# Optimization experiments

Measured on AMD Instinct MI355X. Metric: run time of the kernel, lower is better.

Reference implementation:

```python
import jax, jax.numpy as jnp
import numpy as np

NEG = -100000.0  # matches torch masked_fill constant

def setup_inputs() -> dict:
    key = jax.random.key(0)
    k1, k2, k3, k4 = jax.random.split(key, 4)
    B, T, D, H, S = 8, 2048, 1024, 8, 128
    features = jax.random.normal(k1, (B, T, D), dtype=jnp.float32)
    begins = jax.random.randint(k2, (B, S), 0, 2016, dtype=jnp.int64)
    widths = jax.random.randint(k3, (B, S), 1, 33, dtype=jnp.int64)
    ends = jnp.minimum(begins + widths, T)
    key_w = jax.random.normal(k4, (H, D), dtype=jnp.float32) / np.sqrt(D)
    key_b = jnp.zeros((H,), dtype=jnp.float32)
    return {"features": features, "begins": begins, "ends": ends,
            "key_w": key_w, "key_b": key_b}


def reference(features, begins, ends, key_w, key_b):
    # features: [B, T, D]; begins/ends: [B, S]
    B, T, D = features.shape
    H = key_w.shape[0]
    S = begins.shape[1]
    pos = jnp.arange(T)  # [T]
    # span mask [B, S, T]
    mask = (begins[..., None] <= pos) & (pos < ends[..., None])
    # key projection: [B, T, H]
    logits = jnp.einsum('btd,hd->bth', features, key_w) + key_b
    # masked softmax over T per (batch, span, head): [B, S, T, H]
    masked = jnp.where(mask[..., None], logits[:, None, :, :], NEG)
    weights = jax.nn.softmax(masked, axis=-2)
    # values = features reshaped to heads: [B, T, H, D//H]
    values = features.reshape(B, T, H, D // H)
    res = jnp.einsum('bthd,bsth->bshd', values, weights)  # [B, S, H, D//H]
    return res.reshape(B, S, D)
```

## Files before the change

kernel.cpp:

```cpp
#include <hip/hip_runtime.h>

#define B_  8
#define T_  2048
#define D_  1024
#define H_  8
#define S_  128

__global__ __launch_bounds__(256) void logits_kernel(
    const float* __restrict__ feat,
    const float* __restrict__ kw,
    const float* __restrict__ kb,
    float* __restrict__ logits)
{
    const int wave = threadIdx.x >> 6;
    const int lane = threadIdx.x & 63;
    const int row0 = (blockIdx.x * 4 + wave) * 8;

    float acc[64];
#pragma unroll
    for (int j = 0; j < 64; ++j) acc[j] = 0.f;

#pragma unroll
    for (int c = 0; c < 4; ++c) {
        float4 kf[H_];
#pragma unroll
        for (int h = 0; h < H_; ++h)
            kf[h] = *(const float4*)(kw + h * D_ + c * 256 + lane * 4);
#pragma unroll
        for (int r = 0; r < 8; ++r) {
            float4 fv = *(const float4*)(feat + (size_t)(row0 + r) * D_ + c * 256 + lane * 4);
#pragma unroll
            for (int h = 0; h < H_; ++h)
                acc[r * 8 + h] += fv.x * kf[h].x + fv.y * kf[h].y
                                + fv.z * kf[h].z + fv.w * kf[h].w;
        }
    }

#pragma unroll
    for (int s = 0; s < 6; ++s) {
        const int m = 1 << s;
        const bool hi = (lane >> s) & 1;
#pragma unroll
        for (int j = 0; j < (32 >> s); ++j) {
            float mine  = hi ? acc[2 * j + 1] : acc[2 * j];
            float other = hi ? acc[2 * j]     : acc[2 * j + 1];
            acc[j] = mine + __shfl_xor(other, m, 64);
        }
    }

    logits[(size_t)row0 * H_ + lane] = acc[0] + kb[lane & 7];
}

__global__ __launch_bounds__(256) void pool_kernel(
    const float* __restrict__ feat,
    const int* __restrict__ begins,
    const int* __restrict__ ends,
    const float* __restrict__ logits,
    float* __restrict__ out)
{
    const int bs   = blockIdx.x;
    const int wv   = threadIdx.x >> 6;
    const int lane = threadIdx.x & 63;
    const int b    = bs >> 7;

    const int begin = begins[bs];
    const int width = ends[bs] - begin;
    const size_t row0 = (size_t)b * T_ + begin;

    float4 lv = *(const float4*)(logits + row0 * H_ + lane * 4);
    const int w8 = width * H_;
    float v0 = (4 * lane + 0 < w8) ? lv.x : -1e30f;
    float v1 = (4 * lane + 1 < w8) ? lv.y : -1e30f;
    float v2 = (4 * lane + 2 < w8) ? lv.z : -1e30f;
    float v3 = (4 * lane + 3 < w8) ? lv.w : -1e30f;

    float m0 = v0, m1 = v1, m2 = v2, m3 = v3;
#pragma unroll
    for (int off = 2; off <= 32; off <<= 1) {
        m0 = fmaxf(m0, __shfl_xor(m0, off, 64));
        m1 = fmaxf(m1, __shfl_xor(m1, off, 64));
        m2 = fmaxf(m2, __shfl_xor(m2, off, 64));
        m3 = fmaxf(m3, __shfl_xor(m3, off, 64));
    }

    float e0 = __expf(v0 - m0);
    float e1 = __expf(v1 - m1);
    float e2 = __expf(v2 - m2);
    float e3 = __expf(v3 - m3);
    float s0 = e0, s1 = e1, s2 = e2, s3 = e3;
#pragma unroll
    for (int off = 2; off <= 32; off <<= 1) {
        s0 += __shfl_xor(s0, off, 64);
        s1 += __shfl_xor(s1, off, 64);
        s2 += __shfl_xor(s2, off, 64);
        s3 += __shfl_xor(s3, off, 64);
    }
    const float w0 = e0 / s0, w1 = e1 / s1, w2 = e2 / s2, w3 = e3 / s3;

    const int p = wv >> 1;
    const float wlo = (wv & 1) ? w2 : w0;
    const float whi = (wv & 1) ? w3 : w1;
    const bool hiHalf = (lane >= 32);

    const int colbase = wv * 256 + lane * 4;
    const float* fbase = feat + row0 * D_ + colbase;

    float4 acc = make_float4(0.f, 0.f, 0.f, 0.f);
    const int nch = (width + 7) >> 3;
    for (int ch = 0; ch < nch; ++ch) {
#pragma unroll
        for (int k = 0; k < 8; ++k) {
            const int i = ch * 8 + k;
            const float t0 = __shfl(wlo, 2 * i + p, 64);
            const float t1 = __shfl(whi, 2 * i + p, 64);
            const float wt = hiHalf ? t1 : t0;
            const float4 fv = *(const float4*)(fbase + (size_t)i * D_);
            acc.x += wt * fv.x;
            acc.y += wt * fv.y;
            acc.z += wt * fv.z;
            acc.w += wt * fv.w;
        }
    }

    *(float4*)(out + (size_t)bs * D_ + colbase) = acc;
}

extern "C" void kernel_launch(void* const* d_in, const int* in_sizes, int n_in,
                              void* d_out, int out_size, void* d_ws, size_t ws_size,
                              hipStream_t stream) {
    const float* feat   = (const float*)d_in[0];
    const int*   begins = (const int*)d_in[1];
    const int*   ends   = (const int*)d_in[2];
    const float* kw     = (const float*)d_in[3];
    const float* kb     = (const float*)d_in[4];
    float*       out    = (float*)d_out;
    float* logits = (float*)d_ws;

    logits_kernel<<<(B_ * T_) / 32, 256, 0, stream>>>(feat, kw, kb, logits);
    pool_kernel<<<B_ * S_, 256, 0, stream>>>(feat, begins, ends, logits, out);
}
```

Before: 115.5 us.

## Fuse span logits computation into pooling kernel, computing logits only for span rows

```diff
diff --git a/kernel.cpp b/kernel.cpp
--- a/kernel.cpp
+++ b/kernel.cpp
@@ -6,20 +6,30 @@
 #define H_  8
 #define S_  128
 
-__global__ __launch_bounds__(256) void logits_kernel(
+__global__ __launch_bounds__(256) void pooler_fused(
     const float* __restrict__ feat,
+    const int* __restrict__ begins,
+    const int* __restrict__ ends,
     const float* __restrict__ kw,
     const float* __restrict__ kb,
-    float* __restrict__ logits)
+    float* __restrict__ out)
 {
-    const int wave = threadIdx.x >> 6;
+    const int bs   = blockIdx.x;
+    const int wv   = threadIdx.x >> 6;
     const int lane = threadIdx.x & 63;
-    const int row0 = (blockIdx.x * 4 + wave) * 8;
+    const int b    = bs >> 7;
+
+    const int begin = begins[bs];
+    const int width = ends[bs] - begin;
+    const size_t row0 = (size_t)b * T_ + begin;
+
+    __shared__ __align__(16) float lg[32 * H_];
 
     float acc[64];
 #pragma unroll
     for (int j = 0; j < 64; ++j) acc[j] = 0.f;
 
+    const int r0 = wv * 8;
 #pragma unroll
     for (int c = 0; c < 4; ++c) {
         float4 kf[H_];
@@ -28,7 +38,7 @@
             kf[h] = *(const float4*)(kw + h * D_ + c * 256 + lane * 4);
 #pragma unroll
         for (int r = 0; r < 8; ++r) {
-            float4 fv = *(const float4*)(feat + (size_t)(row0 + r) * D_ + c * 256 + lane * 4);
+            float4 fv = *(const float4*)(feat + (row0 + r0 + r) * D_ + c * 256 + lane * 4);
 #pragma unroll
             for (int h = 0; h < H_; ++h)
                 acc[r * 8 + h] += fv.x * kf[h].x + fv.y * kf[h].y
@@ -48,26 +58,10 @@
         }
     }
 
-    logits[(size_t)row0 * H_ + lane] = acc[0] + kb[lane & 7];
-}
+    lg[wv * 64 + lane] = acc[0] + kb[lane & 7];
+    __syncthreads();
 
-__global__ __launch_bounds__(256) void pool_kernel(
-    const float* __restrict__ feat,
-    const int* __restrict__ begins,
-    const int* __restrict__ ends,
-    const float* __restrict__ logits,
-    float* __restrict__ out)
-{
-    const int bs   = blockIdx.x;
-    const int wv   = threadIdx.x >> 6;
-    const int lane = threadIdx.x & 63;
-    const int b    = bs >> 7;
-
-    const int begin = begins[bs];
-    const int width = ends[bs] - begin;
-    const size_t row0 = (size_t)b * T_ + begin;
-
-    float4 lv = *(const float4*)(logits + row0 * H_ + lane * 4);
+    float4 lv = *(const float4*)&lg[lane * 4];
     const int w8 = width * H_;
     float v0 = (4 * lane + 0 < w8) ? lv.x : -1e30f;
     float v1 = (4 * lane + 1 < w8) ? lv.y : -1e30f;
@@ -105,7 +99,7 @@
     const int colbase = wv * 256 + lane * 4;
     const float* fbase = feat + row0 * D_ + colbase;
 
-    float4 acc = make_float4(0.f, 0.f, 0.f, 0.f);
+    float4 oacc = make_float4(0.f, 0.f, 0.f, 0.f);
     const int nch = (width + 7) >> 3;
     for (int ch = 0; ch < nch; ++ch) {
 #pragma unroll
@@ -115,14 +109,14 @@
             const float t1 = __shfl(whi, 2 * i + p, 64);
             const float wt = hiHalf ? t1 : t0;
             const float4 fv = *(const float4*)(fbase + (size_t)i * D_);
-            acc.x += wt * fv.x;
-            acc.y += wt * fv.y;
-            acc.z += wt * fv.z;
-            acc.w += wt * fv.w;
+            oacc.x += wt * fv.x;
+            oacc.y += wt * fv.y;
+            oacc.z += wt * fv.z;
+            oacc.w += wt * fv.w;
         }
     }
 
-    *(float4*)(out + (size_t)bs * D_ + colbase) = acc;
+    *(float4*)(out + (size_t)bs * D_ + colbase) = oacc;
 }
 
 extern "C" void kernel_launch(void* const* d_in, const int* in_sizes, int n_in,
@@ -134,8 +128,7 @@
     const float* kw     = (const float*)d_in[3];
     const float* kb     = (const float*)d_in[4];
     float*       out    = (float*)d_out;
-    float* logits = (float*)d_ws;
+    (void)d_ws; (void)ws_size;
 
-    logits_kernel<<<(B_ * T_) / 32, 256, 0, stream>>>(feat, kw, kb, logits);
-    pool_kernel<<<B_ * S_, 256, 0, stream>>>(feat, begins, ends, logits, out);
+    pooler_fused<<<B_ * S_, 256, 0, stream>>>(feat, begins, ends, kw, kb, out);
 }
```

Result: no change. 116.4 us (+0.8%).

## Stage key weights in LDS and assign one row per wave in logits kernel

Applied to the files above, without the earlier changes.

```diff
diff --git a/kernel.cpp b/kernel.cpp
--- a/kernel.cpp
+++ b/kernel.cpp
@@ -6,49 +6,64 @@
 #define H_  8
 #define S_  128
 
-__global__ __launch_bounds__(256) void logits_kernel(
+__global__ __launch_bounds__(1024) void logits_kernel(
     const float* __restrict__ feat,
     const float* __restrict__ kw,
     const float* __restrict__ kb,
     float* __restrict__ logits)
 {
-    const int wave = threadIdx.x >> 6;
+    const int wv   = threadIdx.x >> 6;
     const int lane = threadIdx.x & 63;
-    const int row0 = (blockIdx.x * 4 + wave) * 8;
+    const int row  = blockIdx.x * 16 + wv;
 
-    float acc[64];
+    __shared__ __align__(16) float kwl[H_ * D_];
+
+    {
+        const float4* src = (const float4*)kw;
+        float4*       dst = (float4*)kwl;
+        dst[threadIdx.x]        = src[threadIdx.x];
+        dst[threadIdx.x + 1024] = src[threadIdx.x + 1024];
+    }
+
+    const float* fr = feat + (size_t)row * D_;
+    float4 fv0 = *(const float4*)(fr +   0 + lane * 4);
+    float4 fv1 = *(const float4*)(fr + 256 + lane * 4);
+    float4 fv2 = *(const float4*)(fr + 512 + lane * 4);
+    float4 fv3 = *(const float4*)(fr + 768 + lane * 4);
+
+    __syncthreads();
+
+    float acc[H_];
 #pragma unroll
-    for (int j = 0; j < 64; ++j) acc[j] = 0.f;
-
-#pragma unroll
-    for (int c = 0; c < 4; ++c) {
-        float4 kf[H_];
-#pragma unroll
-        for (int h = 0; h < H_; ++h)
-            kf[h] = *(const float4*)(kw + h * D_ + c * 256 + lane * 4);
-#pragma unroll
-        for (int r = 0; r < 8; ++r) {
-            float4 fv = *(const float4*)(feat + (size_t)(row0 + r) * D_ + c * 256 + lane * 4);
-#pragma unroll
-            for (int h = 0; h < H_; ++h)
-                acc[r * 8 + h] += fv.x * kf[h].x + fv.y * kf[h].y
-                                + fv.z * kf[h].z + fv.w * kf[h].w;
-        }
+    for (int h = 0; h < H_; ++h) {
+        const float* kh = &kwl[h * D_ + lane * 4];
+        float4 k0 = *(const float4*)(kh +   0);
+        float4 k1 = *(const float4*)(kh + 256);
+        float4 k2 = *(const float4*)(kh + 512);
+        float4 k3 = *(const float4*)(kh + 768);
+        acc[h] = fv0.x * k0.x + fv0.y * k0.y + fv0.z * k0.z + fv0.w * k0.w
+               + fv1.x * k1.x + fv1.y * k1.y + fv1.z * k1.z + fv1.w * k1.w
+               + fv2.x * k2.x + fv2.y * k2.y + fv2.z * k2.z + fv2.w * k2.w
+               + fv3.x * k3.x + fv3.y * k3.y + fv3.z * k3.z + fv3.w * k3.w;
     }
 
 #pragma unroll
-    for (int s = 0; s < 6; ++s) {
+    for (int s = 0; s < 3; ++s) {
         const int m = 1 << s;
         const bool hi = (lane >> s) & 1;
 #pragma unroll
-        for (int j = 0; j < (32 >> s); ++j) {
+        for (int j = 0; j < (4 >> s); ++j) {
             float mine  = hi ? acc[2 * j + 1] : acc[2 * j];
             float other = hi ? acc[2 * j]     : acc[2 * j + 1];
             acc[j] = mine + __shfl_xor(other, m, 64);
         }
     }
+    acc[0] += __shfl_xor(acc[0],  8, 64);
+    acc[0] += __shfl_xor(acc[0], 16, 64);
+    acc[0] += __shfl_xor(acc[0], 32, 64);
 
-    logits[(size_t)row0 * H_ + lane] = acc[0] + kb[lane & 7];
+    if (lane < H_)
+        logits[(size_t)row * H_ + lane] = acc[0] + kb[lane];
 }
 
 __global__ __launch_bounds__(256) void pool_kernel(
@@ -136,6 +151,6 @@
     float*       out    = (float*)d_out;
     float* logits = (float*)d_ws;
 
-    logits_kernel<<<(B_ * T_) / 32, 256, 0, stream>>>(feat, kw, kb, logits);
+    logits_kernel<<<1024, 1024, 0, stream>>>(feat, kw, kb, logits);
     pool_kernel<<<B_ * S_, 256, 0, stream>>>(feat, begins, ends, logits, out);
 }
```

Measured after the change: 113.1 us. 1.02x faster.
